# Optimization experiments

Hardware: AMD Instinct MI355X
Metric: run time of the kernel (lower is better)

The kernel has to match this reference:

```python
import jax, jax.numpy as jnp
import numpy as np

B, T, D, H = 4, 2048, 1024, 16
DH = D // H  # head dim = 64
FLOAT_MIN = jnp.finfo(jnp.float32).min


def setup_inputs() -> dict:
    key = jax.random.key(0)
    k1, k2, k3 = jax.random.split(key, 3)
    scale = 1.0 / np.sqrt(D)
    return {
        "x": jax.random.normal(k1, (B, T, D), dtype=jnp.float32),
        "W_qkv": jax.random.normal(k2, (D, 3 * D), dtype=jnp.float32) * scale,
        "b_qkv": jnp.zeros((3 * D,), dtype=jnp.float32),
        "W_out": jax.random.normal(k3, (D, D), dtype=jnp.float32) * scale,
        "b_out": jnp.zeros((D,), dtype=jnp.float32),
        "mask": jnp.ones((B, T, T), dtype=jnp.float32),
    }


def _split_heads(t):
    # [B, T, D] -> [B, H, T, DH]
    b, s, _ = t.shape
    return t.reshape(b, s, H, DH).transpose(0, 2, 1, 3)


def reference(x, W_qkv, b_qkv, W_out, b_out, mask):
    # fused QKV projection (Conv1D kernel-size 1 == per-position dense)
    qkv = jnp.einsum("btd,de->bte", x, W_qkv) + b_qkv
    q, k, v = jnp.split(qkv, 3, axis=-1)
    q = _split_heads(q) * (DH ** -0.5)  # [B, H, T, DH]
    k = _split_heads(k)
    v = _split_heads(v)
    # scores [B, H, Tq, Tk]
    dot = jnp.einsum("bhqd,bhkd->bhqk", q, k)
    m = mask[:, None, :, :]  # expand over heads
    dot = dot * m + (1.0 - m) * FLOAT_MIN
    attn = jax.nn.softmax(dot, axis=-1)
    ctx = jnp.einsum("bhqk,bhkd->bhqd", attn, v)  # [B, H, T, DH]
    combined = ctx.transpose(0, 2, 1, 3).reshape(x.shape[0], x.shape[1], D)
    out = jnp.einsum("btd,de->bte", combined, W_out) + b_out
    return out
```

## Files before the change

kernel.cpp:

```cpp
#include <hip/hip_runtime.h>

typedef short bf16x8 __attribute__((ext_vector_type(8)));
typedef float f32x4 __attribute__((ext_vector_type(4)));
typedef float f32x16 __attribute__((ext_vector_type(16)));
typedef unsigned short u16x8 __attribute__((ext_vector_type(8)));

#define DEVI __device__ __forceinline__

static constexpr int T_ = 2048;

DEVI unsigned short f2bf(float f) {
  unsigned int x = __builtin_bit_cast(unsigned int, f);
  x += 0x7fffu + ((x >> 16) & 1u);
  return (unsigned short)(x >> 16);
}

DEVI unsigned int cvtpk(float lo, float hi2) {
  unsigned int r;
  asm("v_cvt_pk_bf16_f32 %0, %1, %2" : "=v"(r) : "v"(lo), "v"(hi2));
  return r;
}

DEVI float exp2_raw(float x) {
  float r;
  asm("v_exp_f32 %0, %1" : "=v"(r) : "v"(x));
  return r;
}

DEVI bf16x8 mkfrag(unsigned a, unsigned b, unsigned c, unsigned d) {
  union { unsigned u[4]; bf16x8 v; } x;
  x.u[0] = a; x.u[1] = b; x.u[2] = c; x.u[3] = d;
  return x.v;
}

DEVI void gl2lds16(const void* g, const void* l) {
  __builtin_amdgcn_global_load_lds(
      (const __attribute__((address_space(1))) void*)g,
      (__attribute__((address_space(3))) void*)l, 16, 0, 0);
}

__global__ __launch_bounds__(256) void k_cvt_bf16(const float* __restrict__ in,
                                                  unsigned short* __restrict__ out) {
  size_t i = ((size_t)blockIdx.x * 256 + threadIdx.x) * 8;
  float4 a = *(const float4*)(in + i);
  float4 b = *(const float4*)(in + i + 4);
  u16x8 o;
  o[0] = f2bf(a.x); o[1] = f2bf(a.y); o[2] = f2bf(a.z); o[3] = f2bf(a.w);
  o[4] = f2bf(b.x); o[5] = f2bf(b.y); o[6] = f2bf(b.z); o[7] = f2bf(b.w);
  *(u16x8*)(out + i) = o;
}

__global__ __launch_bounds__(256) void k_mask_scan(const uint4* __restrict__ m,
                                                   unsigned int* __restrict__ flag) {
  const unsigned int ONE = 0x3f800000u;
  size_t i0 = ((size_t)blockIdx.x * 256 + threadIdx.x) * 8;
  bool ok = true;
#pragma unroll
  for (int i = 0; i < 8; ++i) {
    uint4 v = m[i0 + i];
    ok &= (v.x == ONE) & (v.y == ONE) & (v.z == ONE) & (v.w == ONE);
  }
  if (!ok) atomicAnd(flag, 0u);
}

template <int R, int C>
__global__ __launch_bounds__(256) void k_transpose_cvt(const float* __restrict__ in,
                                                       unsigned short* __restrict__ out) {
  __shared__ unsigned short t[64][65];
  const int c0 = blockIdx.x * 64, r0 = blockIdx.y * 64;
  const int cc = threadIdx.x & 63, r4 = threadIdx.x >> 6;
#pragma unroll
  for (int i = 0; i < 16; ++i) {
    int rr = i * 4 + r4;
    t[rr][cc] = f2bf(in[(size_t)(r0 + rr) * C + c0 + cc]);
  }
  __syncthreads();
#pragma unroll
  for (int i = 0; i < 16; ++i) {
    int rr = i * 4 + r4;
    out[(size_t)(c0 + rr) * R + r0 + cc] = t[cc][rr];
  }
}

__global__ __launch_bounds__(256) void k_transpose_v(const unsigned short* __restrict__ V,
                                                     unsigned short* __restrict__ Vt) {
  __shared__ unsigned short t[64][65];
  const int t0 = blockIdx.x * 64;
  const size_t bh = blockIdx.y;
  const unsigned short* src = V + (bh * T_ + t0) * 64;
  unsigned short* dst = Vt + bh * 64 * T_ + t0;
  const int cc = threadIdx.x & 63, r4 = threadIdx.x >> 6;
#pragma unroll
  for (int i = 0; i < 16; ++i) {
    int rr = i * 4 + r4;
    t[rr][cc] = src[(size_t)rr * 64 + cc];
  }
  __syncthreads();
#pragma unroll
  for (int i = 0; i < 16; ++i) {
    int rr = i * 4 + r4;
    dst[(size_t)rr * T_ + cc] = t[cc][rr];
  }
}

template <int EPI>
__global__ __launch_bounds__(256, 2) void k_gemm(
    const unsigned short* __restrict__ A, const unsigned short* __restrict__ Bt,
    const float* __restrict__ bias,
    unsigned short* __restrict__ qo, unsigned short* __restrict__ ko2,
    unsigned short* __restrict__ vo, float* __restrict__ fo) {
  __shared__ unsigned short As[2][128 * 32];
  __shared__ unsigned short Bs[2][128 * 32];
  const int tid = threadIdx.x;
  const int lane = tid & 63, w = tid >> 6;
  const int wr = w >> 1, wc = w & 1;
  const int g = lane >> 4, c0 = lane & 15;
  const int m0 = blockIdx.y * 128, n0 = blockIdx.x * 128;

  f32x4 acc[4][4] = {};

  const int s0 = tid, s1 = tid + 256;
  const int ar0 = s0 >> 2, ac0 = (s0 & 3) ^ ((ar0 >> 1) & 3);
  const int ar1 = s1 >> 2, ac1 = (s1 & 3) ^ ((ar1 >> 1) & 3);
  const int ldsb0 = w * 512, ldsb1 = w * 512 + 2048;

  const unsigned short* Ar0 = A + (size_t)(m0 + ar0) * 1024 + ac0 * 8;
  const unsigned short* Ar1 = A + (size_t)(m0 + ar1) * 1024 + ac1 * 8;
  const unsigned short* Br0 = Bt + (size_t)(n0 + ar0) * 1024 + ac0 * 8;
  const unsigned short* Br1 = Bt + (size_t)(n0 + ar1) * 1024 + ac1 * 8;

  auto stage = [&](int buf, int kt) {
    const int ke = kt * 32;
    gl2lds16(Ar0 + ke, &As[buf][ldsb0]);
    gl2lds16(Ar1 + ke, &As[buf][ldsb1]);
    gl2lds16(Br0 + ke, &Bs[buf][ldsb0]);
    gl2lds16(Br1 + ke, &Bs[buf][ldsb1]);
  };

  stage(0, 0);
  __syncthreads();
  int cur = 0;
  for (int kt = 0; kt < 32; ++kt) {
    if (kt + 1 < 32) stage(cur ^ 1, kt + 1);
    bf16x8 af[4], bfv[4];
#pragma unroll
    for (int mf = 0; mf < 4; ++mf) {
      int row = wr * 64 + mf * 16 + c0;
      int ch = g ^ ((row >> 1) & 3);
      af[mf] = *(const bf16x8*)&As[cur][row * 32 + ch * 8];
    }
#pragma unroll
    for (int nf = 0; nf < 4; ++nf) {
      int row = wc * 64 + nf * 16 + c0;
      int ch = g ^ ((row >> 1) & 3);
      bfv[nf] = *(const bf16x8*)&Bs[cur][row * 32 + ch * 8];
    }
#pragma unroll
    for (int mf = 0; mf < 4; ++mf)
#pragma unroll
      for (int nf = 0; nf < 4; ++nf)
        acc[mf][nf] = __builtin_amdgcn_mfma_f32_16x16x32_bf16(af[mf], bfv[nf], acc[mf][nf], 0, 0, 0);
    __syncthreads();
    cur ^= 1;
  }

#pragma unroll
  for (int mf = 0; mf < 4; ++mf) {
#pragma unroll
    for (int nf = 0; nf < 4; ++nf) {
      const int n = n0 + wc * 64 + nf * 16 + c0;
      const float bv = bias[n];
#pragma unroll
      for (int r = 0; r < 4; ++r) {
        const int m = m0 + wr * 64 + mf * 16 + g * 4 + r;
        float v = acc[mf][nf][r] + bv;
        if constexpr (EPI == 0) {
          const int sel = n >> 10, hd = n & 1023;
          const int h = hd >> 6, d = hd & 63;
          const int b = m >> 11, t = m & 2047;
          const size_t off = ((size_t)((b * 16 + h) * 2048 + t)) * 64 + d;
          if (sel == 0)       qo[off] = f2bf(v * 0.125f);
          else if (sel == 1)  ko2[off] = f2bf(v);
          else                vo[off] = f2bf(v);
        } else {
          fo[(size_t)m * 1024 + n] = v;
        }
      }
    }
  }
}

__global__ __launch_bounds__(256, 4) void k_attn(
    const unsigned short* __restrict__ Q, const unsigned short* __restrict__ Kg_,
    const unsigned short* __restrict__ Vt, const float* __restrict__ mask,
    const unsigned int* __restrict__ maskflag,
    unsigned short* __restrict__ ctx) {
  __shared__ unsigned short Ks[2][64 * 64];
  __shared__ unsigned short Vs[2][64 * 64];
  const int tid = threadIdx.x, lane = tid & 63, w = tid >> 6;
  const int q = lane & 31, hi = lane >> 5;

  const int flat = blockIdx.x + 16 * blockIdx.y + 256 * blockIdx.z;
  const int work = (flat & 7) * 128 + (flat >> 3);
  const int qb = work & 15;
  const int bh_i = work >> 4;
  const int h = bh_i & 15, b = bh_i >> 4;
  const int t0 = qb * 128;
  const size_t bh = (size_t)bh_i;

  const unsigned short* Qg = Q + (bh * 2048 + t0 + w * 32 + q) * 64;
  const unsigned short* Kg = Kg_ + bh * 2048 * 64;
  const unsigned short* Vg = Vt + bh * 64 * 2048;
  const float* Mg = mask + (size_t)b * 2048 * 2048;
  const bool allones = (*maskflag != 0u);

  bf16x8 qf[4];
#pragma unroll
  for (int kd = 0; kd < 4; ++kd)
    qf[kd] = *(const bf16x8*)(Qg + kd * 16 + hi * 8);

  f32x16 ot[2] = {};
  float mrun = -__builtin_inff(), lrun = 0.f;

  const int s0 = tid, s1 = tid + 256;
  const int kr0 = s0 >> 3, kc0 = (s0 & 7) ^ (kr0 & 7);
  const int kr1 = s1 >> 3, kc1 = (s1 & 7) ^ (kr1 & 7);
  const int ldsb0 = w * 512, ldsb1 = w * 512 + 2048;

  auto stageKV = [&](int buf, int kt) {
    gl2lds16(Kg + (size_t)(kt * 64 + kr0) * 64 + kc0 * 8, &Ks[buf][ldsb0]);
    gl2lds16(Kg + (size_t)(kt * 64 + kr1) * 64 + kc1 * 8, &Ks[buf][ldsb1]);
    gl2lds16(Vg + (size_t)kr0 * 2048 + kt * 64 + kc0 * 8, &Vs[buf][ldsb0]);
    gl2lds16(Vg + (size_t)kr1 * 2048 + kt * 64 + kc1 * 8, &Vs[buf][ldsb1]);
  };

  stageKV(0, 0);
  __syncthreads();
  int cur = 0;
  const float MINF = -3.402823466e38f;
  const float L2E = 1.4426950408889634f;

  for (int kt = 0; kt < 32; ++kt) {
    if (kt + 1 < 32) stageKV(cur ^ 1, kt + 1);

    f32x16 st[2] = {};
#pragma unroll
    for (int mt2 = 0; mt2 < 2; ++mt2) {
#pragma unroll
      for (int kd = 0; kd < 4; ++kd) {
        const int row = mt2 * 32 + q;
        const int ch = (2 * kd + hi) ^ (row & 7);
        bf16x8 kf = *(const bf16x8*)&Ks[cur][row * 64 + ch * 8];
        st[mt2] = __builtin_amdgcn_mfma_f32_32x32x16_bf16(kf, qf[kd], st[mt2], 0, 0, 0);
      }
    }

    if (!allones) {
      const int qg = t0 + w * 32 + q;
#pragma unroll
      for (int mt2 = 0; mt2 < 2; ++mt2)
#pragma unroll
        for (int r = 0; r < 16; ++r) {
          const int kg = kt * 64 + mt2 * 32 + (r & 3) + 8 * (r >> 2) + 4 * hi;
          const float mv = Mg[(size_t)qg * 2048 + kg];
          st[mt2][r] = st[mt2][r] * mv + (1.f - mv) * MINF;
        }
    }

    float t8[8];
#pragma unroll
    for (int i = 0; i < 8; ++i)
      t8[i] = fmaxf(fmaxf(st[0][i], st[0][i + 8]), fmaxf(st[1][i], st[1][i + 8]));
    float t4a = fmaxf(t8[0], t8[4]), t4b = fmaxf(t8[1], t8[5]);
    float t4c = fmaxf(t8[2], t8[6]), t4d = fmaxf(t8[3], t8[7]);
    float tmax = fmaxf(fmaxf(t4a, t4b), fmaxf(t4c, t4d));
    tmax = fmaxf(tmax, __shfl_xor(tmax, 32));
    const bool defer = (__all(tmax <= mrun + 8.f) != 0);
    float alpha = 1.f;
    if (!defer) {
      const float mnew = fmaxf(mrun, tmax);
      alpha = exp2_raw((mrun - mnew) * L2E);
      mrun = mnew;
    }
    const float mL2 = mrun * L2E;
#pragma unroll
    for (int mt2 = 0; mt2 < 2; ++mt2)
#pragma unroll
      for (int i = 0; i < 16; ++i)
        st[mt2][i] = exp2_raw(st[mt2][i] * L2E - mL2);
    float s8[8];
#pragma unroll
    for (int i = 0; i < 8; ++i)
      s8[i] = (st[0][i] + st[0][i + 8]) + (st[1][i] + st[1][i + 8]);
    float s4a = s8[0] + s8[4], s4b = s8[1] + s8[5];
    float s4c = s8[2] + s8[6], s4d = s8[3] + s8[7];
    float ps = (s4a + s4b) + (s4c + s4d);
    ps += __shfl_xor(ps, 32);
    lrun = lrun * alpha + ps;
    if (!defer) {
#pragma unroll
      for (int dt = 0; dt < 2; ++dt)
#pragma unroll
        for (int i = 0; i < 16; ++i) ot[dt][i] *= alpha;
    }

    bf16x8 pf[4];
#pragma unroll
    for (int mt2 = 0; mt2 < 2; ++mt2) {
      unsigned int pw[8];
#pragma unroll
      for (int i = 0; i < 8; ++i) pw[i] = cvtpk(st[mt2][2 * i], st[mt2][2 * i + 1]);
      const unsigned int e0 = __shfl_xor(hi ? pw[0] : pw[2], 32);
      const unsigned int e1 = __shfl_xor(hi ? pw[1] : pw[3], 32);
      const unsigned int e2 = __shfl_xor(hi ? pw[4] : pw[6], 32);
      const unsigned int e3 = __shfl_xor(hi ? pw[5] : pw[7], 32);
      pf[2 * mt2]     = hi ? mkfrag(e0, e1, pw[2], pw[3]) : mkfrag(pw[0], pw[1], e0, e1);
      pf[2 * mt2 + 1] = hi ? mkfrag(e2, e3, pw[6], pw[7]) : mkfrag(pw[4], pw[5], e2, e3);
    }

#pragma unroll
    for (int dt = 0; dt < 2; ++dt) {
#pragma unroll
      for (int kt2 = 0; kt2 < 4; ++kt2) {
        const int row = dt * 32 + q;
        const int ch = (2 * kt2 + hi) ^ (row & 7);
        bf16x8 vf = *(const bf16x8*)&Vs[cur][row * 64 + ch * 8];
        ot[dt] = __builtin_amdgcn_mfma_f32_32x32x16_bf16(vf, pf[kt2], ot[dt], 0, 0, 0);
      }
    }

    __syncthreads();
    cur ^= 1;
  }

  const int qg = t0 + w * 32 + q;
  const float rl = 1.f / lrun;
  unsigned short* cp = ctx + ((size_t)b * 2048 + qg) * 1024 + h * 64;
#pragma unroll
  for (int dt = 0; dt < 2; ++dt) {
#pragma unroll
    for (int rg = 0; rg < 4; ++rg) {
      const int d0 = dt * 32 + rg * 8 + hi * 4;
      ushort4 o;
      o.x = f2bf(ot[dt][rg * 4 + 0] * rl);
      o.y = f2bf(ot[dt][rg * 4 + 1] * rl);
      o.z = f2bf(ot[dt][rg * 4 + 2] * rl);
      o.w = f2bf(ot[dt][rg * 4 + 3] * rl);
      *(ushort4*)(cp + d0) = o;
    }
  }
}

extern "C" void kernel_launch(void* const* d_in, const int* in_sizes, int n_in,
                              void* d_out, int out_size, void* d_ws, size_t ws_size,
                              hipStream_t stream) {
  (void)in_sizes; (void)n_in; (void)out_size; (void)ws_size;
  const float* x    = (const float*)d_in[0];
  const float* Wqkv = (const float*)d_in[1];
  const float* bqkv = (const float*)d_in[2];
  const float* Wout = (const float*)d_in[3];
  const float* bout = (const float*)d_in[4];
  const float* mask = (const float*)d_in[5];
  float* out = (float*)d_out;
  char* ws = (char*)d_ws;

  const size_t SZ_BTD = (size_t)8192 * 1024 * 2;
  unsigned short* xb  = (unsigned short*)(ws);
  unsigned short* Wqt = (unsigned short*)(ws + SZ_BTD);
  unsigned short* Wot = (unsigned short*)(ws + SZ_BTD + 6291456);
  unsigned short* Qb  = (unsigned short*)(ws + SZ_BTD + 8388608);
  unsigned short* Kb  = (unsigned short*)(ws + SZ_BTD + 8388608 + SZ_BTD);
  unsigned short* Vb  = (unsigned short*)(ws + SZ_BTD + 8388608 + 2 * SZ_BTD);
  unsigned short* Vtb = (unsigned short*)(ws + SZ_BTD + 8388608 + 3 * SZ_BTD);
  unsigned int* flag  = (unsigned int*)(ws + SZ_BTD + 8388608 + 4 * SZ_BTD);
  unsigned short* ctx = xb;

  hipMemsetAsync(flag, 1, 4, stream);
  k_mask_scan<<<2048, 256, 0, stream>>>((const uint4*)mask, flag);
  k_cvt_bf16<<<4096, 256, 0, stream>>>(x, xb);
  k_transpose_cvt<1024, 3072><<<dim3(48, 16), 256, 0, stream>>>(Wqkv, Wqt);
  k_transpose_cvt<1024, 1024><<<dim3(16, 16), 256, 0, stream>>>(Wout, Wot);
  k_gemm<0><<<dim3(24, 64), 256, 0, stream>>>(xb, Wqt, bqkv, Qb, Kb, Vb, nullptr);
  k_transpose_v<<<dim3(32, 64), 256, 0, stream>>>(Vb, Vtb);
  k_attn<<<dim3(16, 16, 4), 256, 0, stream>>>(Qb, Kb, Vtb, mask, flag, ctx);
  k_gemm<1><<<dim3(8, 64), 256, 0, stream>>>(ctx, Wot, bout, nullptr, nullptr, nullptr, out);
}
```

Baseline: 236.2 us.

## Permute K rows at staging to drop P cross-lane shuffles; add MFMA priority

K rows are loaded into LDS in a permuted order (swz23), so the S=K·Q accumulator layout lines up directly with the B-operand layout needed for P·V. This removes the four cross-half shuffles per tile when building P fragments. The mask index mapping and the max reduction are updated to match the new element order. The change also wraps the MFMA blocks in s_setprio so matrix work gets issue priority, and raises the GEMM occupancy hint to 3 blocks, which may add register pressure or spills.

```diff
diff --git a/kernel.cpp b/kernel.cpp
--- a/kernel.cpp
+++ b/kernel.cpp
@@ -25,6 +25,11 @@
   float r;
   asm("v_exp_f32 %0, %1" : "=v"(r) : "v"(x));
   return r;
+}
+
+DEVI int swz23(int r) {
+  const int d = ((r >> 2) ^ (r >> 3)) & 1;
+  return r ^ (d << 2) ^ (d << 3);
 }
 
 DEVI bf16x8 mkfrag(unsigned a, unsigned b, unsigned c, unsigned d) {
@@ -104,7 +109,7 @@
 }
 
 template <int EPI>
-__global__ __launch_bounds__(256, 2) void k_gemm(
+__global__ __launch_bounds__(256, 3) void k_gemm(
     const unsigned short* __restrict__ A, const unsigned short* __restrict__ Bt,
     const float* __restrict__ bias,
     unsigned short* __restrict__ qo, unsigned short* __restrict__ ko2,
@@ -155,11 +160,13 @@
       int ch = g ^ ((row >> 1) & 3);
       bfv[nf] = *(const bf16x8*)&Bs[cur][row * 32 + ch * 8];
     }
+    __builtin_amdgcn_s_setprio(1);
 #pragma unroll
     for (int mf = 0; mf < 4; ++mf)
 #pragma unroll
       for (int nf = 0; nf < 4; ++nf)
         acc[mf][nf] = __builtin_amdgcn_mfma_f32_16x16x32_bf16(af[mf], bfv[nf], acc[mf][nf], 0, 0, 0);
+    __builtin_amdgcn_s_setprio(0);
     __syncthreads();
     cur ^= 1;
   }
@@ -225,11 +232,12 @@
   const int s0 = tid, s1 = tid + 256;
   const int kr0 = s0 >> 3, kc0 = (s0 & 7) ^ (kr0 & 7);
   const int kr1 = s1 >> 3, kc1 = (s1 & 7) ^ (kr1 & 7);
+  const int kp0 = swz23(kr0), kp1 = swz23(kr1);
   const int ldsb0 = w * 512, ldsb1 = w * 512 + 2048;
 
   auto stageKV = [&](int buf, int kt) {
-    gl2lds16(Kg + (size_t)(kt * 64 + kr0) * 64 + kc0 * 8, &Ks[buf][ldsb0]);
-    gl2lds16(Kg + (size_t)(kt * 64 + kr1) * 64 + kc1 * 8, &Ks[buf][ldsb1]);
+    gl2lds16(Kg + (size_t)(kt * 64 + kp0) * 64 + kc0 * 8, &Ks[buf][ldsb0]);
+    gl2lds16(Kg + (size_t)(kt * 64 + kp1) * 64 + kc1 * 8, &Ks[buf][ldsb1]);
     gl2lds16(Vg + (size_t)kr0 * 2048 + kt * 64 + kc0 * 8, &Vs[buf][ldsb0]);
     gl2lds16(Vg + (size_t)kr1 * 2048 + kt * 64 + kc1 * 8, &Vs[buf][ldsb1]);
   };
@@ -246,6 +254,7 @@
     f32x16 st[2] = {};
 #pragma unroll
     for (int mt2 = 0; mt2 < 2; ++mt2) {
+      __builtin_amdgcn_s_setprio(1);
 #pragma unroll
       for (int kd = 0; kd < 4; ++kd) {
         const int row = mt2 * 32 + q;
@@ -253,6 +262,7 @@
         bf16x8 kf = *(const bf16x8*)&Ks[cur][row * 64 + ch * 8];
         st[mt2] = __builtin_amdgcn_mfma_f32_32x32x16_bf16(kf, qf[kd], st[mt2], 0, 0, 0);
       }
+      __builtin_amdgcn_s_setprio(0);
     }
 
     if (!allones) {
@@ -261,19 +271,23 @@
       for (int mt2 = 0; mt2 < 2; ++mt2)
 #pragma unroll
         for (int r = 0; r < 16; ++r) {
-          const int kg = kt * 64 + mt2 * 32 + (r & 3) + 8 * (r >> 2) + 4 * hi;
+          const int kg = kt * 64 + mt2 * 32 +
+                         (r & 3) + 4 * ((r >> 2) & 1) + 8 * hi + 16 * (r >> 3);
           const float mv = Mg[(size_t)qg * 2048 + kg];
           st[mt2][r] = st[mt2][r] * mv + (1.f - mv) * MINF;
         }
     }
 
-    float t8[8];
-#pragma unroll
-    for (int i = 0; i < 8; ++i)
-      t8[i] = fmaxf(fmaxf(st[0][i], st[0][i + 8]), fmaxf(st[1][i], st[1][i + 8]));
-    float t4a = fmaxf(t8[0], t8[4]), t4b = fmaxf(t8[1], t8[5]);
-    float t4c = fmaxf(t8[2], t8[6]), t4d = fmaxf(t8[3], t8[7]);
-    float tmax = fmaxf(fmaxf(t4a, t4b), fmaxf(t4c, t4d));
+    float g4[8];
+#pragma unroll
+    for (int i = 0; i < 4; ++i) {
+      g4[i]     = fmaxf(fmaxf(fmaxf(st[0][4 * i], st[0][4 * i + 1]), st[0][4 * i + 2]), st[0][4 * i + 3]);
+      g4[i + 4] = fmaxf(fmaxf(fmaxf(st[1][4 * i], st[1][4 * i + 1]), st[1][4 * i + 2]), st[1][4 * i + 3]);
+    }
+    float r1 = fmaxf(fmaxf(g4[0], g4[1]), g4[2]);
+    float r2 = fmaxf(fmaxf(g4[3], g4[4]), g4[5]);
+    float r3 = fmaxf(fmaxf(g4[6], g4[7]), r1);
+    float tmax = fmaxf(r2, r3);
     tmax = fmaxf(tmax, __shfl_xor(tmax, 32));
     const bool defer = (__all(tmax <= mrun + 8.f) != 0);
     float alpha = 1.f;
@@ -310,16 +324,13 @@
       unsigned int pw[8];
 #pragma unroll
       for (int i = 0; i < 8; ++i) pw[i] = cvtpk(st[mt2][2 * i], st[mt2][2 * i + 1]);
-      const unsigned int e0 = __shfl_xor(hi ? pw[0] : pw[2], 32);
-      const unsigned int e1 = __shfl_xor(hi ? pw[1] : pw[3], 32);
-      const unsigned int e2 = __shfl_xor(hi ? pw[4] : pw[6], 32);
-      const unsigned int e3 = __shfl_xor(hi ? pw[5] : pw[7], 32);
-      pf[2 * mt2]     = hi ? mkfrag(e0, e1, pw[2], pw[3]) : mkfrag(pw[0], pw[1], e0, e1);
-      pf[2 * mt2 + 1] = hi ? mkfrag(e2, e3, pw[6], pw[7]) : mkfrag(pw[4], pw[5], e2, e3);
+      pf[2 * mt2]     = mkfrag(pw[0], pw[1], pw[2], pw[3]);
+      pf[2 * mt2 + 1] = mkfrag(pw[4], pw[5], pw[6], pw[7]);
     }
 
 #pragma unroll
     for (int dt = 0; dt < 2; ++dt) {
+      __builtin_amdgcn_s_setprio(1);
 #pragma unroll
       for (int kt2 = 0; kt2 < 4; ++kt2) {
         const int row = dt * 32 + q;
@@ -327,6 +338,7 @@
         bf16x8 vf = *(const bf16x8*)&Vs[cur][row * 64 + ch * 8];
         ot[dt] = __builtin_amdgcn_mfma_f32_32x32x16_bf16(vf, pf[kt2], ot[dt], 0, 0, 0);
       }
+      __builtin_amdgcn_s_setprio(0);
     }
 
     __syncthreads();
```

After: 230.8 us. 1.02x faster.
